# Kernel tuning notes

Measured on AMD Instinct MI355X. Metric: run time of the kernel, lower is better.

Reference implementation:

```python
import jax, jax.numpy as jnp
import numpy as np
import math

B, N, E = 256, 512, 2048          # graphs, nodes per graph, edges per graph
EMB = 64                           # emb_sz (must be 64 to match final per-graph matmul with 64-d fc2 output)
NUM_ITEMS, NUM_CATS = 400000, 1000
RATIO = 0.9
EPS = 1e-5


def _bn(x, g, b):
    # BatchNorm1d in training mode: biased batch statistics
    m = x.mean(axis=0)
    v = x.var(axis=0)
    return g * (x - m) * jax.lax.rsqrt(v + EPS) + b


def _graph_conv(x, src, dst, emask, Wr, Wn, b):
    # PyG GraphConv, aggr='add': out_i = lin_root(x_i) + lin_rel(sum_{j->i} x_j) + bias
    msg = jnp.where(emask[:, None], x[src], jnp.zeros((), x.dtype))  # [E_tot, C]
    agg = jnp.zeros_like(x).at[dst].add(msg)
    return agg @ Wn + x @ Wr + b


def _topk_pool(x, src, dst, emask, p, n):
    # TopKPooling: score = x.p/||p||, keep top ceil(ratio*n) per graph, gate with tanh(score)
    k = int(math.ceil(RATIO * n))
    score = x @ p / jnp.linalg.norm(p)                       # [B*n]
    _, idx = jax.lax.top_k(score.reshape(B, n), k)           # [B, k] local indices
    gidx = (idx + (jnp.arange(B) * n)[:, None]).reshape(-1)  # [B*k] global indices
    xk = x[gidx] * jnp.tanh(score[gidx])[:, None]
    # remap edges; edges touching a dropped node become masked-out
    mapping = jnp.full((B * n,), -1, jnp.int32).at[gidx].set(jnp.arange(B * k, dtype=jnp.int32))
    nsrc, ndst = mapping[src], mapping[dst]
    valid = (nsrc >= 0) & (ndst >= 0) & emask
    return xk, jnp.maximum(nsrc, 0), jnp.maximum(ndst, 0), valid, k


def _readout(x, k):
    # uniform graphs: global_max_pool / global_mean_pool via reshape
    xg = x.reshape(B, k, -1)
    return jnp.concatenate([xg.max(axis=1), xg.mean(axis=1)], axis=1)  # [B, 256]


def setup_inputs() -> dict:
    key = jax.random.key(0)
    ks = jax.random.split(key, 32)
    nrm = jax.random.normal
    s = 0.02
    item_id = jax.random.randint(ks[0], (B * N,), 0, NUM_ITEMS)
    cat_id = jax.random.randint(ks[1], (B * N,), 0, NUM_CATS)
    off = (jnp.arange(B, dtype=jnp.int32) * N)[:, None]
    src = (jax.random.randint(ks[2], (B, E), 0, N, dtype=jnp.int32) + off).reshape(-1)
    dst = (jax.random.randint(ks[3], (B, E), 0, N, dtype=jnp.int32) + off).reshape(-1)
    d = dict(
        item_id=item_id, cat_id=cat_id, src=src, dst=dst,
        emb_item=nrm(ks[4], (NUM_ITEMS, EMB)) * s,
        emb_cat=nrm(ks[5], (NUM_CATS, EMB)) * s,
        W1r=nrm(ks[6], (2 * EMB, 128)) * s, W1n=nrm(ks[7], (2 * EMB, 128)) * s, b1=jnp.zeros(128), p1=nrm(ks[8], (128,)),
        W2r=nrm(ks[9], (128, 128)) * s, W2n=nrm(ks[10], (128, 128)) * s, b2=jnp.zeros(128), p2=nrm(ks[11], (128,)),
        W3r=nrm(ks[12], (128, 128)) * s, W3n=nrm(ks[13], (128, 128)) * s, b3=jnp.zeros(128), p3=nrm(ks[14], (128,)),
        fc1_W=nrm(ks[15], (256, 128)) * s, fc1_b=jnp.zeros(128), bn1_g=jnp.ones(128), bn1_b=jnp.zeros(128),
        fc2_W=nrm(ks[16], (128, 64)) * s, fc2_b=jnp.zeros(64), bn2_g=jnp.ones(64), bn2_b=jnp.zeros(64),
    )
    return d


def reference(item_id, cat_id, src, dst, emb_item, emb_cat,
              W1r, W1n, b1, p1, W2r, W2n, b2, p2, W3r, W3n, b3, p3,
              fc1_W, fc1_b, bn1_g, bn1_b, fc2_W, fc2_b, bn2_g, bn2_b):
    e_item = emb_item[item_id]                               # [B*N, 64]
    e_cat = emb_cat[cat_id]                                  # [B*N, 64]
    x = jnp.concatenate([e_item, e_cat], axis=1)             # [B*N, 128]
    emask = jnp.ones(src.shape, bool)

    x = jax.nn.relu(_graph_conv(x, src, dst, emask, W1r, W1n, b1))
    x, src, dst, emask, k1 = _topk_pool(x, src, dst, emask, p1, N)
    x1 = _readout(x, k1)

    x = jax.nn.relu(_graph_conv(x, src, dst, emask, W2r, W2n, b2))
    x, src, dst, emask, k2 = _topk_pool(x, src, dst, emask, p2, k1)
    x2 = _readout(x, k2)

    x = jax.nn.relu(_graph_conv(x, src, dst, emask, W3r, W3n, b3))
    x, src, dst, emask, k3 = _topk_pool(x, src, dst, emask, p3, k2)
    x3 = _readout(x, k3)

    g = x1 + x2 + x3                                         # [B, 256]
    g = jax.nn.relu(_bn(g @ fc1_W + fc1_b, bn1_g, bn1_b))    # fc1
    g = jax.nn.relu(_bn(g @ fc2_W + fc2_b, bn2_g, bn2_b))    # fc2
    # dropout is identity in eval; original applies relu again after dropout
    g = jax.nn.relu(g)                                       # [B, 64]
    # per-graph matmul loop: out[n] = <emb_item[n], g[graph_of_n]>; uniform graphs -> einsum
    out = jnp.einsum('bnd,bd->bn', e_item.reshape(B, N, EMB), g).reshape(-1)
    return jax.nn.sigmoid(out)                               # [B*N]
```

## Files before the change

kernel.cpp:

```cpp
#include <hip/hip_runtime.h>
#include <hip/hip_bf16.h>
#include <math.h>


#define TOTAL_NODES 131072
#define NUM_GRAPHS  256
#define NODES_PER_G 512
#define E_TOTAL     524288
#define EPG         2048
#define FDIM        128
#define EMBD        64

typedef __bf16 bf16x8 __attribute__((ext_vector_type(8)));
typedef float  f32x4  __attribute__((ext_vector_type(4)));

static __device__ __forceinline__ f32x4 mfma16(bf16x8 a, bf16x8 b, f32x4 c) {
  return __builtin_amdgcn_mfma_f32_16x16x32_bf16(a, b, c, 0, 0, 0);
}

static inline size_t align256(size_t x) { return (x + 255) & ~size_t(255); }

__global__ __launch_bounds__(256) void gather_embed_k(
    const int* __restrict__ item_id, const int* __restrict__ cat_id,
    const float* __restrict__ emb_item, const float* __restrict__ emb_cat,
    float* __restrict__ x, int total)
{
  int i = blockIdx.x * 256 + threadIdx.x;
  int node = i >> 5, part = i & 31;
  if (node >= total) return;
  float4 v;
  if (part < 16) {
    v = *(const float4*)&emb_item[(size_t)item_id[node] * EMBD + part * 4];
  } else {
    v = *(const float4*)&emb_cat[(size_t)cat_id[node] * EMBD + (part - 16) * 4];
  }
  *(float4*)&x[(size_t)node * FDIM + part * 4] = v;
}

__global__ __launch_bounds__(256) void wprep_k(
    const float* __restrict__ w0, const float* __restrict__ w1,
    const float* __restrict__ w2, const float* __restrict__ w3,
    const float* __restrict__ w4, const float* __restrict__ w5,
    __bf16* __restrict__ wout)
{
  const float* ws[6] = {w0, w1, w2, w3, w4, w5};
  int mat = blockIdx.y;
  int idx = blockIdx.x * 256 + threadIdx.x;
  int n = idx >> 7, k = idx & 127;
  float v = ws[mat][k * FDIM + n];
  __bf16 h = (__bf16)v;
  __bf16 l = (__bf16)(v - (float)h);
  __bf16* base = wout + (size_t)mat * 2 * 16384;
  base[idx] = h;
  base[16384 + idx] = l;
}

__global__ __launch_bounds__(128) void pnorm3_k(
    const float* __restrict__ p1, const float* __restrict__ p2,
    const float* __restrict__ p3, float* __restrict__ nrm)
{
  __shared__ float ss[128];
  const float* ps[3] = {p1, p2, p3};
  int t = threadIdx.x;
  for (int m = 0; m < 3; ++m) {
    float v = ps[m][t];
    ss[t] = v * v;
    __syncthreads();
    for (int s = 64; s > 0; s >>= 1) {
      if (t < s) ss[t] += ss[t + s];
      __syncthreads();
    }
    if (t == 0) nrm[m] = sqrtf(ss[0]);
    __syncthreads();
  }
}

__global__ __launch_bounds__(512) void csr_build_k(
    const int* __restrict__ src_in, const int* __restrict__ dst_in,
    const int* __restrict__ mapping,
    const int* __restrict__ sel_,
    const float* __restrict__ gates_,
    int* __restrict__ src_out, int* __restrict__ dst_out,
    int2* __restrict__ slot_pack, int* __restrict__ counts,
    int* __restrict__ offs, int n_new)
{
  __shared__ int hist[512];
  __shared__ int scan[512];
  __shared__ int cursor[512];
  const int g = blockIdx.x, t = threadIdx.x;
  const int ebase = g * EPG;
  const int nbase = g * n_new;
  hist[t] = 0;
  __syncthreads();
  int ls[4], ld[4];
#pragma unroll
  for (int i = 0; i < 4; ++i) {
    int e = ebase + t + i * 512;
    int s = src_in[e], d = dst_in[e];
    if (mapping) {
      s = (s >= 0) ? mapping[s] : -1;
      d = (d >= 0) ? mapping[d] : -1;
      if (s < 0 || d < 0) { s = -1; d = -1; }
    }
    src_out[e] = s; dst_out[e] = d;
    ls[i] = (s >= 0) ? (s - nbase) : -1;
    ld[i] = (d >= 0) ? (d - nbase) : -1;
    if (ld[i] >= 0) atomicAdd(&hist[ld[i]], 1);
  }
  __syncthreads();
  int v = (t < n_new) ? hist[t] : 0;
  scan[t] = v;
  __syncthreads();
  for (int dlt = 1; dlt < 512; dlt <<= 1) {
    int add = (t >= dlt) ? scan[t - dlt] : 0;
    __syncthreads();
    scan[t] += add;
    __syncthreads();
  }
  if (t < n_new) {
    int excl = scan[t] - v;
    counts[nbase + t] = v;
    offs[nbase + t] = g * EPG + excl;
    cursor[t] = excl;
  }
  __syncthreads();
#pragma unroll
  for (int i = 0; i < 4; ++i) {
    if (ld[i] >= 0) {
      int pos = atomicAdd(&cursor[ld[i]], 1);
      int sg = nbase + ls[i];
      int oldr = sel_ ? sel_[sg] : sg;
      float gt = gates_ ? gates_[sg] : 1.0f;
      slot_pack[ebase + pos] = make_int2(oldr, __float_as_int(gt));
    }
  }
}

__global__ __launch_bounds__(256) void gather_direct_k(
    const float* __restrict__ x, const int2* __restrict__ slot_pack,
    const int* __restrict__ off, const int* __restrict__ counts,
    float* __restrict__ agg, int M)
{
  int i = blockIdx.x * 256 + threadIdx.x;
  int node = i >> 5, lane = i & 31;
  if (node >= M) return;
  int deg = counts[node];
  int base = off[node];
  float4 a = make_float4(0.f, 0.f, 0.f, 0.f);
  for (int d = 0; d < deg; ++d) {
    int2 sp = slot_pack[base + d];
    float gt = __int_as_float(sp.y);
    float4 v = *(const float4*)&x[(size_t)sp.x * FDIM + lane * 4];
    a.x += gt * v.x; a.y += gt * v.y; a.z += gt * v.z; a.w += gt * v.w;
  }
  *(float4*)&agg[(size_t)node * FDIM + lane * 4] = a;
}

__global__ __launch_bounds__(256) void conv_mfma_k(
    const float* __restrict__ Asrc, const int* __restrict__ sel,
    const float* __restrict__ gates,
    const __bf16* __restrict__ W1hl,
    const float* __restrict__ A2,
    const __bf16* __restrict__ W2hl,
    const float* __restrict__ bias, const float* __restrict__ p,
    const float* __restrict__ nrm, float* __restrict__ C,
    float* __restrict__ score, int M)
{
  __shared__ __bf16 Wh[128 * 72];
  __shared__ __bf16 Wl[128 * 72];

  const int tid  = threadIdx.x;
  const int lane = tid & 63;
  const int w    = tid >> 6;
  const int row0 = blockIdx.x * 128;
  const int l15  = lane & 15;
  const int lg   = lane >> 4;

  f32x4 acc[2][8];
#pragma unroll
  for (int rf = 0; rf < 2; ++rf)
#pragma unroll
    for (int cf = 0; cf < 8; ++cf) acc[rf][cf] = (f32x4){0.f, 0.f, 0.f, 0.f};

  const int grow0 = row0 + w * 32 + l15;
  const int grow1 = grow0 + 16;

  for (int pass = 0; pass < 2; ++pass) {
    const float* __restrict__ A = pass ? A2 : Asrc;
    const __bf16* __restrict__ Whl = pass ? W2hl : W1hl;
    const bool use_sel = (pass == 0) && (sel != nullptr);
    int srow0 = use_sel ? sel[grow0] : grow0;
    int srow1 = use_sel ? sel[grow1] : grow1;
    float gt0 = use_sel ? gates[grow0] : 1.0f;
    float gt1 = use_sel ? gates[grow1] : 1.0f;

    for (int half = 0; half < 2; ++half) {
      const int k0 = half * 64;
      __syncthreads();
      for (int v = tid; v < 1024; v += 256) {
        int c = v >> 3, chn = (v & 7) * 8;
        *(bf16x8*)&Wh[c * 72 + chn] = *(const bf16x8*)&Whl[c * 128 + k0 + chn];
        *(bf16x8*)&Wl[c * 72 + chn] = *(const bf16x8*)&Whl[16384 + c * 128 + k0 + chn];
      }
      __syncthreads();

      bf16x8 ah[2][2], al[2][2];
#pragma unroll
      for (int rf = 0; rf < 2; ++rf) {
        int srow = rf ? srow1 : srow0;
        float gt = rf ? gt1 : gt0;
#pragma unroll
        for (int kc = 0; kc < 2; ++kc) {
          const float* ap = &A[(size_t)srow * FDIM + k0 + kc * 32 + lg * 8];
          float4 u0 = *(const float4*)ap;
          float4 u1 = *(const float4*)(ap + 4);
          float av[8] = {u0.x, u0.y, u0.z, u0.w, u1.x, u1.y, u1.z, u1.w};
#pragma unroll
          for (int j = 0; j < 8; ++j) {
            float vv = av[j] * gt;
            __bf16 h = (__bf16)vv;
            ah[rf][kc][j] = h;
            al[rf][kc][j] = (__bf16)(vv - (float)h);
          }
        }
      }
#pragma unroll
      for (int kc = 0; kc < 2; ++kc) {
        const int koff = kc * 32 + lg * 8;
#pragma unroll
        for (int cf = 0; cf < 8; ++cf) {
          const int bo = (cf * 16 + l15) * 72 + koff;
          bf16x8 bh = *(const bf16x8*)&Wh[bo];
          bf16x8 bl = *(const bf16x8*)&Wl[bo];
          acc[0][cf] = mfma16(ah[0][kc], bh, acc[0][cf]);
          acc[0][cf] = mfma16(ah[0][kc], bl, acc[0][cf]);
          acc[0][cf] = mfma16(al[0][kc], bh, acc[0][cf]);
          acc[1][cf] = mfma16(ah[1][kc], bh, acc[1][cf]);
          acc[1][cf] = mfma16(ah[1][kc], bl, acc[1][cf]);
          acc[1][cf] = mfma16(al[1][kc], bh, acc[1][cf]);
        }
      }
    }
  }

  const float nv = nrm[0];
  float bv[8], pv[8];
#pragma unroll
  for (int cf = 0; cf < 8; ++cf) {
    int col = cf * 16 + l15;
    bv[cf] = bias[col];
    pv[cf] = p[col];
  }
#pragma unroll
  for (int rf = 0; rf < 2; ++rf) {
#pragma unroll
    for (int j = 0; j < 4; ++j) {
      int row = row0 + w * 32 + rf * 16 + lg * 4 + j;
      float* crow = &C[(size_t)row * FDIM];
      float rsv = 0.f;
#pragma unroll
      for (int cf = 0; cf < 8; ++cf) {
        float val = acc[rf][cf][j] + bv[cf];
        val = fmaxf(val, 0.f);
        crow[cf * 16 + l15] = val;
        rsv += val * pv[cf];
      }
      rsv += __shfl_xor(rsv, 1, 16);
      rsv += __shfl_xor(rsv, 2, 16);
      rsv += __shfl_xor(rsv, 4, 16);
      rsv += __shfl_xor(rsv, 8, 16);
      if (l15 == 0) score[row] = rsv / nv;
    }
  }
}

__global__ __launch_bounds__(512) void topk_sort_k(
    const float* __restrict__ score, int n_old, int k_new,
    int* __restrict__ sel, int* __restrict__ mapping, float* __restrict__ gates)
{
  __shared__ float sv[512];
  __shared__ int   si[512];
  int b = blockIdx.x, t = threadIdx.x;
  sv[t] = (t < n_old) ? -score[(size_t)b * n_old + t] : 3.0e38f;
  si[t] = t;
  __syncthreads();
  for (int k = 2; k <= 512; k <<= 1) {
    for (int j = k >> 1; j > 0; j >>= 1) {
      int ixj = t ^ j;
      if (ixj > t) {
        bool up = ((t & k) == 0);
        float a = sv[t], c = sv[ixj];
        if ((a > c) == up) {
          sv[t] = c; sv[ixj] = a;
          int tmp = si[t]; si[t] = si[ixj]; si[ixj] = tmp;
        }
      }
      __syncthreads();
    }
  }
  if (t < n_old) {
    int old_g = b * n_old + si[t];
    if (t < k_new) {
      sel[b * k_new + t] = old_g;
      mapping[old_g] = b * k_new + t;
      gates[b * k_new + t] = tanhf(-sv[t]);
    } else {
      mapping[old_g] = -1;
    }
  }
}

__global__ __launch_bounds__(256) void readout_k(
    const float* __restrict__ x, const int* __restrict__ sel,
    const float* __restrict__ gates, float* __restrict__ g, int k)
{
  __shared__ float lmx[32 * 36];
  __shared__ float lsm[32 * 36];
  const int b = blockIdx.x, ch = blockIdx.y;
  const int c0 = ch * 32;
  const int tid = threadIdx.x;
  const int lane = tid & 7;
  const int slot = tid >> 3;
  float4 mx = make_float4(-3.0e38f, -3.0e38f, -3.0e38f, -3.0e38f);
  float4 sm = make_float4(0.f, 0.f, 0.f, 0.f);
  for (int n = slot; n < k; n += 32) {
    int node = b * k + n;
    int old = sel[node];
    float gate = gates[node];
    float4 v = *(const float4*)&x[(size_t)old * FDIM + c0 + lane * 4];
    v.x *= gate; v.y *= gate; v.z *= gate; v.w *= gate;
    mx.x = fmaxf(mx.x, v.x); mx.y = fmaxf(mx.y, v.y);
    mx.z = fmaxf(mx.z, v.z); mx.w = fmaxf(mx.w, v.w);
    sm.x += v.x; sm.y += v.y; sm.z += v.z; sm.w += v.w;
  }
  float* pm = &lmx[slot * 36 + lane * 4];
  float* ps = &lsm[slot * 36 + lane * 4];
  pm[0] = mx.x; pm[1] = mx.y; pm[2] = mx.z; pm[3] = mx.w;
  ps[0] = sm.x; ps[1] = sm.y; ps[2] = sm.z; ps[3] = sm.w;
  __syncthreads();
  for (int s = 16; s > 0; s >>= 1) {
    if (slot < s) {
#pragma unroll
      for (int j = 0; j < 4; ++j) {
        int a = slot * 36 + lane * 4 + j;
        int bb = (slot + s) * 36 + lane * 4 + j;
        lmx[a] = fmaxf(lmx[a], lmx[bb]);
        lsm[a] += lsm[bb];
      }
    }
    __syncthreads();
  }
  if (slot == 0) {
    float inv_k = 1.f / (float)k;
#pragma unroll
    for (int j = 0; j < 4; ++j) {
      int c = c0 + lane * 4 + j;
      g[b * 256 + c]       += lmx[lane * 4 + j];
      g[b * 256 + 128 + c] += lsm[lane * 4 + j] * inv_k;
    }
  }
}

__global__ __launch_bounds__(256) void head1_k(
    const float* __restrict__ g, const float* __restrict__ W,
    const float* __restrict__ bias, const float* __restrict__ gamma,
    const float* __restrict__ beta, float* __restrict__ h1)
{
  __shared__ float wsl[256 * 8];
  __shared__ float rsum[256 * 9];
  __shared__ float rsq[256 * 9];
  const int c0 = blockIdx.x * 8;
  const int t = threadIdx.x;
#pragma unroll
  for (int j = 0; j < 8; ++j) wsl[t * 8 + j] = W[t * 128 + c0 + j];
  __syncthreads();
  float acc[8] = {0.f, 0.f, 0.f, 0.f, 0.f, 0.f, 0.f, 0.f};
  const float* grow = &g[t * 256];
#pragma unroll
  for (int k = 0; k < 256; k += 4) {
    float4 gv = *(const float4*)&grow[k];
#pragma unroll
    for (int j = 0; j < 8; ++j) {
      acc[j] += gv.x * wsl[(k + 0) * 8 + j] + gv.y * wsl[(k + 1) * 8 + j]
              + gv.z * wsl[(k + 2) * 8 + j] + gv.w * wsl[(k + 3) * 8 + j];
    }
  }
#pragma unroll
  for (int j = 0; j < 8; ++j) {
    acc[j] += bias[c0 + j];
    rsum[t * 9 + j] = acc[j];
    rsq[t * 9 + j] = acc[j] * acc[j];
  }
  __syncthreads();
  for (int s = 128; s > 0; s >>= 1) {
    if (t < s) {
#pragma unroll
      for (int j = 0; j < 8; ++j) {
        rsum[t * 9 + j] += rsum[(t + s) * 9 + j];
        rsq[t * 9 + j]  += rsq[(t + s) * 9 + j];
      }
    }
    __syncthreads();
  }
#pragma unroll
  for (int j = 0; j < 8; ++j) {
    float m = rsum[j] * (1.f / 256.f);
    float var = rsq[j] * (1.f / 256.f) - m * m;
    float o = gamma[c0 + j] * (acc[j] - m) * rsqrtf(var + 1e-5f) + beta[c0 + j];
    h1[t * 128 + c0 + j] = fmaxf(o, 0.f);
  }
}

__global__ __launch_bounds__(256) void head2_k(
    const float* __restrict__ h1, const float* __restrict__ W,
    const float* __restrict__ bias, const float* __restrict__ gamma,
    const float* __restrict__ beta, float* __restrict__ h2)
{
  __shared__ float wsl[128 * 8];
  __shared__ float rsum[256 * 9];
  __shared__ float rsq[256 * 9];
  const int c0 = blockIdx.x * 8;
  const int t = threadIdx.x;
  if (t < 128) {
#pragma unroll
    for (int j = 0; j < 8; ++j) wsl[t * 8 + j] = W[t * 64 + c0 + j];
  }
  __syncthreads();
  float acc[8] = {0.f, 0.f, 0.f, 0.f, 0.f, 0.f, 0.f, 0.f};
  const float* hrow = &h1[t * 128];
#pragma unroll
  for (int k = 0; k < 128; k += 4) {
    float4 gv = *(const float4*)&hrow[k];
#pragma unroll
    for (int j = 0; j < 8; ++j) {
      acc[j] += gv.x * wsl[(k + 0) * 8 + j] + gv.y * wsl[(k + 1) * 8 + j]
              + gv.z * wsl[(k + 2) * 8 + j] + gv.w * wsl[(k + 3) * 8 + j];
    }
  }
#pragma unroll
  for (int j = 0; j < 8; ++j) {
    acc[j] += bias[c0 + j];
    rsum[t * 9 + j] = acc[j];
    rsq[t * 9 + j] = acc[j] * acc[j];
  }
  __syncthreads();
  for (int s = 128; s > 0; s >>= 1) {
    if (t < s) {
#pragma unroll
      for (int j = 0; j < 8; ++j) {
        rsum[t * 9 + j] += rsum[(t + s) * 9 + j];
        rsq[t * 9 + j]  += rsq[(t + s) * 9 + j];
      }
    }
    __syncthreads();
  }
#pragma unroll
  for (int j = 0; j < 8; ++j) {
    float m = rsum[j] * (1.f / 256.f);
    float var = rsq[j] * (1.f / 256.f) - m * m;
    float o = gamma[c0 + j] * (acc[j] - m) * rsqrtf(var + 1e-5f) + beta[c0 + j];
    h2[t * 64 + c0 + j] = fmaxf(o, 0.f);
  }
}

__global__ __launch_bounds__(256) void final_k(
    const int* __restrict__ item_id, const float* __restrict__ emb_item,
    const float* __restrict__ g2, float* __restrict__ out, int total)
{
  int nid = blockIdx.x * 256 + threadIdx.x;
  if (nid >= total) return;
  int b = nid >> 9;
  const float* e = &emb_item[(size_t)item_id[nid] * EMBD];
  const float* gg = &g2[(size_t)b * 64];
  float s = 0.f;
#pragma unroll
  for (int j = 0; j < 64; j += 4) {
    float4 a = *(const float4*)&e[j];
    float4 c = *(const float4*)&gg[j];
    s += a.x * c.x + a.y * c.y + a.z * c.z + a.w * c.w;
  }
  out[nid] = 1.f / (1.f + expf(-s));
}

extern "C" void kernel_launch(void* const* d_in, const int* in_sizes, int n_in,
                              void* d_out, int out_size, void* d_ws, size_t ws_size,
                              hipStream_t stream)
{
  const int*   item_id  = (const int*)  d_in[0];
  const int*   cat_id   = (const int*)  d_in[1];
  const int*   src_in   = (const int*)  d_in[2];
  const int*   dst_in   = (const int*)  d_in[3];
  const float* emb_item = (const float*)d_in[4];
  const float* emb_cat  = (const float*)d_in[5];
  const float* W1r = (const float*)d_in[6];
  const float* W1n = (const float*)d_in[7];
  const float* b1  = (const float*)d_in[8];
  const float* p1  = (const float*)d_in[9];
  const float* W2r = (const float*)d_in[10];
  const float* W2n = (const float*)d_in[11];
  const float* b2  = (const float*)d_in[12];
  const float* p2  = (const float*)d_in[13];
  const float* W3r = (const float*)d_in[14];
  const float* W3n = (const float*)d_in[15];
  const float* b3  = (const float*)d_in[16];
  const float* p3  = (const float*)d_in[17];
  const float* fc1_W = (const float*)d_in[18];
  const float* fc1_b = (const float*)d_in[19];
  const float* bn1_g = (const float*)d_in[20];
  const float* bn1_b = (const float*)d_in[21];
  const float* fc2_W = (const float*)d_in[22];
  const float* fc2_b = (const float*)d_in[23];
  const float* bn2_g = (const float*)d_in[24];
  const float* bn2_b = (const float*)d_in[25];
  float* out = (float*)d_out;

  const int TN = TOTAL_NODES;
  const int E  = E_TOTAL;
  const int k1 = 461, k2 = 415, k3 = 374;
  const int M1 = TN;
  const int M2 = NUM_GRAPHS * k1;
  const int M3 = NUM_GRAPHS * k2;

  char* ws = (char*)d_ws;
  size_t off = 0;
  auto carve = [&](size_t bytes) { char* p = ws + off; off += align256(bytes); return p; };
  float*  buf0   = (float*) carve((size_t)TN * FDIM * 4);
  float*  buf1   = (float*) carve((size_t)TN * FDIM * 4);
  float*  score  = (float*) carve((size_t)TN * 4);
  int*    sel    = (int*)   carve((size_t)TN * 4);
  int*    mapping= (int*)   carve((size_t)TN * 4);
  float*  gates  = (float*) carve((size_t)TN * 4);
  int*    srcw   = (int*)   carve((size_t)E * 4);
  int*    dstw   = (int*)   carve((size_t)E * 4);
  int*    counts = (int*)   carve((size_t)TN * 4);
  int*    offs   = (int*)   carve((size_t)TN * 4);
  int2*   slotp  = (int2*)  carve((size_t)E * 8);
  __bf16* wbuf   = (__bf16*)carve(6 * 2 * 16384 * 2);
  float*  g      = (float*) carve(256 * 256 * 4);
  float*  h1     = (float*) carve(256 * 128 * 4);
  float*  h2     = (float*) carve(256 * 64 * 4);
  float*  nrm    = (float*) carve(256);
  if (off > ws_size) return;

  dim3 b256(256);
  auto blocks = [](long long work, int bs) { return dim3((unsigned)((work + bs - 1) / bs)); };

  const __bf16* W1r_hl = wbuf + 0 * 2 * 16384;
  const __bf16* W1n_hl = wbuf + 1 * 2 * 16384;
  const __bf16* W2r_hl = wbuf + 2 * 2 * 16384;
  const __bf16* W2n_hl = wbuf + 3 * 2 * 16384;
  const __bf16* W3r_hl = wbuf + 4 * 2 * 16384;
  const __bf16* W3n_hl = wbuf + 5 * 2 * 16384;

  hipMemsetAsync(g, 0, 256 * 256 * 4, stream);
  wprep_k<<<dim3(64, 6), b256, 0, stream>>>(W1r, W1n, W2r, W2n, W3r, W3n, wbuf);
  pnorm3_k<<<dim3(1), dim3(128), 0, stream>>>(p1, p2, p3, nrm);
  gather_embed_k<<<blocks((long long)TN * 32, 256), b256, 0, stream>>>(
      item_id, cat_id, emb_item, emb_cat, buf0, TN);

  csr_build_k<<<dim3(NUM_GRAPHS), dim3(512), 0, stream>>>(
      src_in, dst_in, nullptr, nullptr, nullptr,
      srcw, dstw, slotp, counts, offs, NODES_PER_G);
  gather_direct_k<<<blocks((long long)M1 * 32, 256), b256, 0, stream>>>(
      buf0, slotp, offs, counts, buf1, M1);
  conv_mfma_k<<<dim3(M1 / 128), b256, 0, stream>>>(
      buf0, nullptr, nullptr, W1r_hl, buf1, W1n_hl, b1, p1, nrm + 0, buf0, score, M1);
  topk_sort_k<<<dim3(NUM_GRAPHS), dim3(512), 0, stream>>>(
      score, NODES_PER_G, k1, sel, mapping, gates);
  readout_k<<<dim3(NUM_GRAPHS, 4), b256, 0, stream>>>(buf0, sel, gates, g, k1);

  csr_build_k<<<dim3(NUM_GRAPHS), dim3(512), 0, stream>>>(
      srcw, dstw, mapping, sel, gates,
      srcw, dstw, slotp, counts, offs, k1);
  gather_direct_k<<<blocks((long long)M2 * 32, 256), b256, 0, stream>>>(
      buf0, slotp, offs, counts, buf1, M2);
  conv_mfma_k<<<dim3(M2 / 128), b256, 0, stream>>>(
      buf0, sel, gates, W2r_hl, buf1, W2n_hl, b2, p2, nrm + 1, buf1, score, M2);
  topk_sort_k<<<dim3(NUM_GRAPHS), dim3(512), 0, stream>>>(
      score, k1, k2, sel, mapping, gates);
  readout_k<<<dim3(NUM_GRAPHS, 4), b256, 0, stream>>>(buf1, sel, gates, g, k2);

  csr_build_k<<<dim3(NUM_GRAPHS), dim3(512), 0, stream>>>(
      srcw, dstw, mapping, sel, gates,
      srcw, dstw, slotp, counts, offs, k2);
  gather_direct_k<<<blocks((long long)M3 * 32, 256), b256, 0, stream>>>(
      buf1, slotp, offs, counts, buf0, M3);
  conv_mfma_k<<<dim3(M3 / 128), b256, 0, stream>>>(
      buf1, sel, gates, W3r_hl, buf0, W3n_hl, b3, p3, nrm + 2, buf0, score, M3);
  topk_sort_k<<<dim3(NUM_GRAPHS), dim3(512), 0, stream>>>(
      score, k2, k3, sel, mapping, gates);
  readout_k<<<dim3(NUM_GRAPHS, 4), b256, 0, stream>>>(buf0, sel, gates, g, k3);

  head1_k<<<dim3(16), b256, 0, stream>>>(g, fc1_W, fc1_b, bn1_g, bn1_b, h1);
  head2_k<<<dim3(8), b256, 0, stream>>>(h1, fc2_W, fc2_b, bn2_g, bn2_b, h2);

  final_k<<<blocks(TN, 256), b256, 0, stream>>>(item_id, emb_item, h2, out, TN);
}
```

Before: 409.0 us.

## Fuse top-k, edge remap/CSR build and readout into one per-graph pool kernel

Merges the top-k sort, the next-level CSR construction and the max/mean readout into a single per-graph pool kernel. The node mapping and gates now stay in shared memory instead of a global mapping array. The first CSR build is specialised to skip the mapping logic. The final kernel reads item embeddings from the already gathered node features instead of re-gathering through item_id. This cuts kernel launches and global round trips, at the cost of extra feature buffers and a larger shared-memory footprint per block.

```diff
diff --git a/kernel.cpp b/kernel.cpp
--- a/kernel.cpp
+++ b/kernel.cpp
@@ -75,64 +75,50 @@
   }
 }
 
-__global__ __launch_bounds__(512) void csr_build_k(
+__global__ __launch_bounds__(512) void csr_build1_k(
     const int* __restrict__ src_in, const int* __restrict__ dst_in,
-    const int* __restrict__ mapping,
-    const int* __restrict__ sel_,
-    const float* __restrict__ gates_,
     int* __restrict__ src_out, int* __restrict__ dst_out,
-    int2* __restrict__ slot_pack, int* __restrict__ counts,
-    int* __restrict__ offs, int n_new)
+    int2* __restrict__ slot_pack, int* __restrict__ counts, int* __restrict__ offs)
 {
   __shared__ int hist[512];
-  __shared__ int scan[512];
-  __shared__ int cursor[512];
-  const int g = blockIdx.x, t = threadIdx.x;
-  const int ebase = g * EPG;
-  const int nbase = g * n_new;
+  __shared__ int scn[512];
+  __shared__ int cur[512];
+  const int b = blockIdx.x, t = threadIdx.x;
+  const int ebase = b * EPG;
+  const int nbase = b * NODES_PER_G;
   hist[t] = 0;
   __syncthreads();
-  int ls[4], ld[4];
+  int so[4], ld[4];
 #pragma unroll
   for (int i = 0; i < 4; ++i) {
     int e = ebase + t + i * 512;
-    int s = src_in[e], d = dst_in[e];
-    if (mapping) {
-      s = (s >= 0) ? mapping[s] : -1;
-      d = (d >= 0) ? mapping[d] : -1;
-      if (s < 0 || d < 0) { s = -1; d = -1; }
-    }
+    int s = src_in[e] - nbase;
+    int d = dst_in[e] - nbase;
     src_out[e] = s; dst_out[e] = d;
-    ls[i] = (s >= 0) ? (s - nbase) : -1;
-    ld[i] = (d >= 0) ? (d - nbase) : -1;
-    if (ld[i] >= 0) atomicAdd(&hist[ld[i]], 1);
-  }
-  __syncthreads();
-  int v = (t < n_new) ? hist[t] : 0;
-  scan[t] = v;
-  __syncthreads();
-  for (int dlt = 1; dlt < 512; dlt <<= 1) {
-    int add = (t >= dlt) ? scan[t - dlt] : 0;
-    __syncthreads();
-    scan[t] += add;
-    __syncthreads();
-  }
-  if (t < n_new) {
-    int excl = scan[t] - v;
+    so[i] = s; ld[i] = d;
+    atomicAdd(&hist[d], 1);
+  }
+  __syncthreads();
+  int v = hist[t];
+  scn[t] = v;
+  __syncthreads();
+  for (int dd = 1; dd < 512; dd <<= 1) {
+    int add = (t >= dd) ? scn[t - dd] : 0;
+    __syncthreads();
+    scn[t] += add;
+    __syncthreads();
+  }
+  {
+    int excl = scn[t] - v;
     counts[nbase + t] = v;
-    offs[nbase + t] = g * EPG + excl;
-    cursor[t] = excl;
+    offs[nbase + t] = ebase + excl;
+    cur[t] = excl;
   }
   __syncthreads();
 #pragma unroll
   for (int i = 0; i < 4; ++i) {
-    if (ld[i] >= 0) {
-      int pos = atomicAdd(&cursor[ld[i]], 1);
-      int sg = nbase + ls[i];
-      int oldr = sel_ ? sel_[sg] : sg;
-      float gt = gates_ ? gates_[sg] : 1.0f;
-      slot_pack[ebase + pos] = make_int2(oldr, __float_as_int(gt));
-    }
+    int pos = atomicAdd(&cur[ld[i]], 1);
+    slot_pack[ebase + pos] = make_int2(nbase + so[i], __float_as_int(1.0f));
   }
 }
 
@@ -274,21 +260,33 @@
   }
 }
 
-__global__ __launch_bounds__(512) void topk_sort_k(
-    const float* __restrict__ score, int n_old, int k_new,
-    int* __restrict__ sel, int* __restrict__ mapping, float* __restrict__ gates)
+__global__ __launch_bounds__(512) void pool_k(
+    const float* __restrict__ score, const float* __restrict__ x,
+    int n_old, int k_new,
+    int* __restrict__ sel, float* __restrict__ gates,
+    int* __restrict__ src_e, int* __restrict__ dst_e,
+    int2* __restrict__ slot_pack, int* __restrict__ counts,
+    int* __restrict__ offs, float* __restrict__ g)
 {
   __shared__ float sv[512];
   __shared__ int   si[512];
-  int b = blockIdx.x, t = threadIdx.x;
-  sv[t] = (t < n_old) ? -score[(size_t)b * n_old + t] : 3.0e38f;
+  __shared__ int   map_[512];
+  __shared__ float gl[512];
+  __shared__ int   hist[512];
+  __shared__ int   scn[512];
+  __shared__ int   cur[512];
+  __shared__ float rmx[4 * 128];
+  __shared__ float rsm[4 * 128];
+  const int b = blockIdx.x, t = threadIdx.x;
+  const int nbase = b * n_old;
+  sv[t] = (t < n_old) ? -score[nbase + t] : 3.0e38f;
   si[t] = t;
   __syncthreads();
-  for (int k = 2; k <= 512; k <<= 1) {
-    for (int j = k >> 1; j > 0; j >>= 1) {
+  for (int kk = 2; kk <= 512; kk <<= 1) {
+    for (int j = kk >> 1; j > 0; j >>= 1) {
       int ixj = t ^ j;
       if (ixj > t) {
-        bool up = ((t & k) == 0);
+        bool up = ((t & kk) == 0);
         float a = sv[t], c = sv[ixj];
         if ((a > c) == up) {
           sv[t] = c; sv[ixj] = a;
@@ -299,64 +297,79 @@
     }
   }
   if (t < n_old) {
-    int old_g = b * n_old + si[t];
+    int o = si[t];
     if (t < k_new) {
-      sel[b * k_new + t] = old_g;
-      mapping[old_g] = b * k_new + t;
-      gates[b * k_new + t] = tanhf(-sv[t]);
+      float gt = tanhf(-sv[t]);
+      sel[b * k_new + t] = nbase + o;
+      gates[b * k_new + t] = gt;
+      gl[t] = gt;
+      map_[o] = t;
     } else {
-      mapping[old_g] = -1;
-    }
-  }
-}
-
-__global__ __launch_bounds__(256) void readout_k(
-    const float* __restrict__ x, const int* __restrict__ sel,
-    const float* __restrict__ gates, float* __restrict__ g, int k)
-{
-  __shared__ float lmx[32 * 36];
-  __shared__ float lsm[32 * 36];
-  const int b = blockIdx.x, ch = blockIdx.y;
-  const int c0 = ch * 32;
-  const int tid = threadIdx.x;
-  const int lane = tid & 7;
-  const int slot = tid >> 3;
-  float4 mx = make_float4(-3.0e38f, -3.0e38f, -3.0e38f, -3.0e38f);
-  float4 sm = make_float4(0.f, 0.f, 0.f, 0.f);
-  for (int n = slot; n < k; n += 32) {
-    int node = b * k + n;
-    int old = sel[node];
-    float gate = gates[node];
-    float4 v = *(const float4*)&x[(size_t)old * FDIM + c0 + lane * 4];
-    v.x *= gate; v.y *= gate; v.z *= gate; v.w *= gate;
-    mx.x = fmaxf(mx.x, v.x); mx.y = fmaxf(mx.y, v.y);
-    mx.z = fmaxf(mx.z, v.z); mx.w = fmaxf(mx.w, v.w);
-    sm.x += v.x; sm.y += v.y; sm.z += v.z; sm.w += v.w;
-  }
-  float* pm = &lmx[slot * 36 + lane * 4];
-  float* ps = &lsm[slot * 36 + lane * 4];
-  pm[0] = mx.x; pm[1] = mx.y; pm[2] = mx.z; pm[3] = mx.w;
-  ps[0] = sm.x; ps[1] = sm.y; ps[2] = sm.z; ps[3] = sm.w;
-  __syncthreads();
-  for (int s = 16; s > 0; s >>= 1) {
-    if (slot < s) {
-#pragma unroll
-      for (int j = 0; j < 4; ++j) {
-        int a = slot * 36 + lane * 4 + j;
-        int bb = (slot + s) * 36 + lane * 4 + j;
-        lmx[a] = fmaxf(lmx[a], lmx[bb]);
-        lsm[a] += lsm[bb];
-      }
-    }
-    __syncthreads();
-  }
-  if (slot == 0) {
-    float inv_k = 1.f / (float)k;
-#pragma unroll
-    for (int j = 0; j < 4; ++j) {
-      int c = c0 + lane * 4 + j;
-      g[b * 256 + c]       += lmx[lane * 4 + j];
-      g[b * 256 + 128 + c] += lsm[lane * 4 + j] * inv_k;
+      map_[o] = -1;
+    }
+  }
+  __syncthreads();
+  if (slot_pack) {
+    hist[t] = 0;
+    __syncthreads();
+    const int ebase = b * EPG;
+    int so[4], ls[4], ld[4];
+#pragma unroll
+    for (int i = 0; i < 4; ++i) {
+      int e = ebase + t + i * 512;
+      int s = src_e[e], d = dst_e[e];
+      so[i] = s;
+      int ns = (s >= 0) ? map_[s] : -1;
+      int nd = (d >= 0) ? map_[d] : -1;
+      if (ns < 0 || nd < 0) { ns = -1; nd = -1; }
+      src_e[e] = ns; dst_e[e] = nd;
+      ls[i] = ns; ld[i] = nd;
+      if (nd >= 0) atomicAdd(&hist[nd], 1);
+    }
+    __syncthreads();
+    int v = (t < k_new) ? hist[t] : 0;
+    scn[t] = v;
+    __syncthreads();
+    for (int dd = 1; dd < 512; dd <<= 1) {
+      int add = (t >= dd) ? scn[t - dd] : 0;
+      __syncthreads();
+      scn[t] += add;
+      __syncthreads();
+    }
+    if (t < k_new) {
+      int excl = scn[t] - v;
+      counts[b * k_new + t] = v;
+      offs[b * k_new + t] = ebase + excl;
+      cur[t] = excl;
+    }
+    __syncthreads();
+#pragma unroll
+    for (int i = 0; i < 4; ++i) {
+      if (ld[i] >= 0) {
+        int pos = atomicAdd(&cur[ld[i]], 1);
+        slot_pack[ebase + pos] = make_int2(nbase + so[i], __float_as_int(gl[ls[i]]));
+      }
+    }
+  }
+  {
+    const int col = t & 127;
+    const int slot = t >> 7;
+    float mx = -3.0e38f, sm = 0.f;
+    for (int n = slot; n < k_new; n += 4) {
+      int old = nbase + si[n];
+      float v = x[(size_t)old * FDIM + col] * gl[n];
+      mx = fmaxf(mx, v);
+      sm += v;
+    }
+    rmx[slot * 128 + col] = mx;
+    rsm[slot * 128 + col] = sm;
+    __syncthreads();
+    if (slot == 0) {
+      float m0 = fmaxf(fmaxf(rmx[col], rmx[128 + col]),
+                       fmaxf(rmx[256 + col], rmx[384 + col]));
+      float s0 = rsm[col] + rsm[128 + col] + rsm[256 + col] + rsm[384 + col];
+      g[b * 256 + col]       += m0;
+      g[b * 256 + 128 + col] += s0 / (float)k_new;
     }
   }
 }
@@ -464,13 +477,13 @@
 }
 
 __global__ __launch_bounds__(256) void final_k(
-    const int* __restrict__ item_id, const float* __restrict__ emb_item,
-    const float* __restrict__ g2, float* __restrict__ out, int total)
+    const float* __restrict__ x0, const float* __restrict__ g2,
+    float* __restrict__ out, int total)
 {
   int nid = blockIdx.x * 256 + threadIdx.x;
   if (nid >= total) return;
   int b = nid >> 9;
-  const float* e = &emb_item[(size_t)item_id[nid] * EMBD];
+  const float* e = &x0[(size_t)nid * FDIM];
   const float* gg = &g2[(size_t)b * 64];
   float s = 0.f;
 #pragma unroll
@@ -524,11 +537,12 @@
   char* ws = (char*)d_ws;
   size_t off = 0;
   auto carve = [&](size_t bytes) { char* p = ws + off; off += align256(bytes); return p; };
-  float*  buf0   = (float*) carve((size_t)TN * FDIM * 4);
-  float*  buf1   = (float*) carve((size_t)TN * FDIM * 4);
+  float*  bufA   = (float*) carve((size_t)TN * FDIM * 4);
+  float*  bufB   = (float*) carve((size_t)TN * FDIM * 4);
+  float*  bufC   = (float*) carve((size_t)TN * FDIM * 4);
+  float*  bufD   = (float*) carve((size_t)TN * FDIM * 4);
   float*  score  = (float*) carve((size_t)TN * 4);
   int*    sel    = (int*)   carve((size_t)TN * 4);
-  int*    mapping= (int*)   carve((size_t)TN * 4);
   float*  gates  = (float*) carve((size_t)TN * 4);
   int*    srcw   = (int*)   carve((size_t)E * 4);
   int*    dstw   = (int*)   carve((size_t)E * 4);
@@ -556,43 +570,36 @@
   wprep_k<<<dim3(64, 6), b256, 0, stream>>>(W1r, W1n, W2r, W2n, W3r, W3n, wbuf);
   pnorm3_k<<<dim3(1), dim3(128), 0, stream>>>(p1, p2, p3, nrm);
   gather_embed_k<<<blocks((long long)TN * 32, 256), b256, 0, stream>>>(
-      item_id, cat_id, emb_item, emb_cat, buf0, TN);
-
-  csr_build_k<<<dim3(NUM_GRAPHS), dim3(512), 0, stream>>>(
-      src_in, dst_in, nullptr, nullptr, nullptr,
-      srcw, dstw, slotp, counts, offs, NODES_PER_G);
+      item_id, cat_id, emb_item, emb_cat, bufA, TN);
+
+  csr_build1_k<<<dim3(NUM_GRAPHS), dim3(512), 0, stream>>>(
+      src_in, dst_in, srcw, dstw, slotp, counts, offs);
   gather_direct_k<<<blocks((long long)M1 * 32, 256), b256, 0, stream>>>(
-      buf0, slotp, offs, counts, buf1, M1);
+      bufA, slotp, offs, counts, bufB, M1);
   conv_mfma_k<<<dim3(M1 / 128), b256, 0, stream>>>(
-      buf0, nullptr, nullptr, W1r_hl, buf1, W1n_hl, b1, p1, nrm + 0, buf0, score, M1);
-  topk_sort_k<<<dim3(NUM_GRAPHS), dim3(512), 0, stream>>>(
-      score, NODES_PER_G, k1, sel, mapping, gates);
-  readout_k<<<dim3(NUM_GRAPHS, 4), b256, 0, stream>>>(buf0, sel, gates, g, k1);
-
-  csr_build_k<<<dim3(NUM_GRAPHS), dim3(512), 0, stream>>>(
-      srcw, dstw, mapping, sel, gates,
-      srcw, dstw, slotp, counts, offs, k1);
+      bufA, nullptr, nullptr, W1r_hl, bufB, W1n_hl, b1, p1, nrm + 0, bufC, score, M1);
+  pool_k<<<dim3(NUM_GRAPHS), dim3(512), 0, stream>>>(
+      score, bufC, NODES_PER_G, k1, sel, gates, srcw, dstw,
+      slotp, counts, offs, g);
+
   gather_direct_k<<<blocks((long long)M2 * 32, 256), b256, 0, stream>>>(
-      buf0, slotp, offs, counts, buf1, M2);
+      bufC, slotp, offs, counts, bufB, M2);
   conv_mfma_k<<<dim3(M2 / 128), b256, 0, stream>>>(
-      buf0, sel, gates, W2r_hl, buf1, W2n_hl, b2, p2, nrm + 1, buf1, score, M2);
-  topk_sort_k<<<dim3(NUM_GRAPHS), dim3(512), 0, stream>>>(
-      score, k1, k2, sel, mapping, gates);
-  readout_k<<<dim3(NUM_GRAPHS, 4), b256, 0, stream>>>(buf1, sel, gates, g, k2);
-
-  csr_build_k<<<dim3(NUM_GRAPHS), dim3(512), 0, stream>>>(
-      srcw, dstw, mapping, sel, gates,
-      srcw, dstw, slotp, counts, offs, k2);
+      bufC, sel, gates, W2r_hl, bufB, W2n_hl, b2, p2, nrm + 1, bufD, score, M2);
+  pool_k<<<dim3(NUM_GRAPHS), dim3(512), 0, stream>>>(
+      score, bufD, k1, k2, sel, gates, srcw, dstw,
+      slotp, counts, offs, g);
+
   gather_direct_k<<<blocks((long long)M3 * 32, 256), b256, 0, stream>>>(
-      buf1, slotp, offs, counts, buf0, M3);
+      bufD, slotp, offs, counts, bufB, M3);
   conv_mfma_k<<<dim3(M3 / 128), b256, 0, stream>>>(
-      buf1, sel, gates, W3r_hl, buf0, W3n_hl, b3, p3, nrm + 2, buf0, score, M3);
-  topk_sort_k<<<dim3(NUM_GRAPHS), dim3(512), 0, stream>>>(
-      score, k2, k3, sel, mapping, gates);
-  readout_k<<<dim3(NUM_GRAPHS, 4), b256, 0, stream>>>(buf0, sel, gates, g, k3);
+      bufD, sel, gates, W3r_hl, bufB, W3n_hl, b3, p3, nrm + 2, bufC, score, M3);
+  pool_k<<<dim3(NUM_GRAPHS), dim3(512), 0, stream>>>(
+      score, bufC, k2, k3, sel, gates, nullptr, nullptr,
+      nullptr, nullptr, nullptr, g);
 
   head1_k<<<dim3(16), b256, 0, stream>>>(g, fc1_W, fc1_b, bn1_g, bn1_b, h1);
   head2_k<<<dim3(8), b256, 0, stream>>>(h1, fc2_W, fc2_b, bn2_g, bn2_b, h2);
 
-  final_k<<<blocks(TN, 256), b256, 0, stream>>>(item_id, emb_item, h2, out, TN);
-}
+  final_k<<<blocks(TN, 256), b256, 0, stream>>>(bufA, h2, out, TN);
+}
```

Result: slower. 494.3 us (+20.9%).

## Fuse neighbor aggregation into conv MFMA kernel and reuse gathered embeddings

Applied to the files above, without the earlier changes.

Removes the separate gather_direct_k kernel and computes the per-node neighbor sum directly inside conv_mfma_k's A-operand load for the neighbor pass, so the aggregated tensor is never written to or re-read from global memory. A third feature buffer is added so each conv reads and writes distinct buffers. The final kernel now reads item embeddings from the already-gathered x0 buffer (first 64 columns) instead of re-gathering from the embedding table. The trade-off is that the neighbor gather now runs twice per row (once for each K half) inside the MFMA kernel, with divergent degree loops that may stall the matrix pipeline.

```diff
diff --git a/kernel.cpp b/kernel.cpp
--- a/kernel.cpp
+++ b/kernel.cpp
@@ -136,32 +136,13 @@
   }
 }
 
-__global__ __launch_bounds__(256) void gather_direct_k(
-    const float* __restrict__ x, const int2* __restrict__ slot_pack,
-    const int* __restrict__ off, const int* __restrict__ counts,
-    float* __restrict__ agg, int M)
-{
-  int i = blockIdx.x * 256 + threadIdx.x;
-  int node = i >> 5, lane = i & 31;
-  if (node >= M) return;
-  int deg = counts[node];
-  int base = off[node];
-  float4 a = make_float4(0.f, 0.f, 0.f, 0.f);
-  for (int d = 0; d < deg; ++d) {
-    int2 sp = slot_pack[base + d];
-    float gt = __int_as_float(sp.y);
-    float4 v = *(const float4*)&x[(size_t)sp.x * FDIM + lane * 4];
-    a.x += gt * v.x; a.y += gt * v.y; a.z += gt * v.z; a.w += gt * v.w;
-  }
-  *(float4*)&agg[(size_t)node * FDIM + lane * 4] = a;
-}
-
 __global__ __launch_bounds__(256) void conv_mfma_k(
     const float* __restrict__ Asrc, const int* __restrict__ sel,
     const float* __restrict__ gates,
-    const __bf16* __restrict__ W1hl,
-    const float* __restrict__ A2,
-    const __bf16* __restrict__ W2hl,
+    const __bf16* __restrict__ Wr_hl,
+    const int2* __restrict__ slotp, const int* __restrict__ offs,
+    const int* __restrict__ counts,
+    const __bf16* __restrict__ Wn_hl,
     const float* __restrict__ bias, const float* __restrict__ p,
     const float* __restrict__ nrm, float* __restrict__ C,
     float* __restrict__ score, int M)
@@ -185,15 +166,15 @@
   const int grow0 = row0 + w * 32 + l15;
   const int grow1 = grow0 + 16;
 
+  const int  srow0 = sel ? sel[grow0] : grow0;
+  const int  srow1 = sel ? sel[grow1] : grow1;
+  const float gt0  = gates ? gates[grow0] : 1.0f;
+  const float gt1  = gates ? gates[grow1] : 1.0f;
+  const int deg0 = counts[grow0], base0 = offs[grow0];
+  const int deg1 = counts[grow1], base1 = offs[grow1];
+
   for (int pass = 0; pass < 2; ++pass) {
-    const float* __restrict__ A = pass ? A2 : Asrc;
-    const __bf16* __restrict__ Whl = pass ? W2hl : W1hl;
-    const bool use_sel = (pass == 0) && (sel != nullptr);
-    int srow0 = use_sel ? sel[grow0] : grow0;
-    int srow1 = use_sel ? sel[grow1] : grow1;
-    float gt0 = use_sel ? gates[grow0] : 1.0f;
-    float gt1 = use_sel ? gates[grow1] : 1.0f;
-
+    const __bf16* __restrict__ Whl = pass ? Wn_hl : Wr_hl;
     for (int half = 0; half < 2; ++half) {
       const int k0 = half * 64;
       __syncthreads();
@@ -207,17 +188,45 @@
       bf16x8 ah[2][2], al[2][2];
 #pragma unroll
       for (int rf = 0; rf < 2; ++rf) {
-        int srow = rf ? srow1 : srow0;
-        float gt = rf ? gt1 : gt0;
-#pragma unroll
-        for (int kc = 0; kc < 2; ++kc) {
-          const float* ap = &A[(size_t)srow * FDIM + k0 + kc * 32 + lg * 8];
+        float av[2][8];
+        if (pass == 0) {
+          int srow = rf ? srow1 : srow0;
+          float gt = rf ? gt1 : gt0;
+          const float* ap = &Asrc[(size_t)srow * FDIM + k0 + lg * 8];
           float4 u0 = *(const float4*)ap;
           float4 u1 = *(const float4*)(ap + 4);
-          float av[8] = {u0.x, u0.y, u0.z, u0.w, u1.x, u1.y, u1.z, u1.w};
+          float4 u2 = *(const float4*)(ap + 32);
+          float4 u3 = *(const float4*)(ap + 36);
+          av[0][0]=gt*u0.x; av[0][1]=gt*u0.y; av[0][2]=gt*u0.z; av[0][3]=gt*u0.w;
+          av[0][4]=gt*u1.x; av[0][5]=gt*u1.y; av[0][6]=gt*u1.z; av[0][7]=gt*u1.w;
+          av[1][0]=gt*u2.x; av[1][1]=gt*u2.y; av[1][2]=gt*u2.z; av[1][3]=gt*u2.w;
+          av[1][4]=gt*u3.x; av[1][5]=gt*u3.y; av[1][6]=gt*u3.z; av[1][7]=gt*u3.w;
+        } else {
+          int deg = rf ? deg1 : deg0;
+          int base = rf ? base1 : base0;
+#pragma unroll
+          for (int kc = 0; kc < 2; ++kc)
+#pragma unroll
+            for (int j = 0; j < 8; ++j) av[kc][j] = 0.f;
+          for (int d = 0; d < deg; ++d) {
+            int2 sp = slotp[base + d];
+            float gt = __int_as_float(sp.y);
+            const float* ap = &Asrc[(size_t)sp.x * FDIM + k0 + lg * 8];
+            float4 u0 = *(const float4*)ap;
+            float4 u1 = *(const float4*)(ap + 4);
+            float4 u2 = *(const float4*)(ap + 32);
+            float4 u3 = *(const float4*)(ap + 36);
+            av[0][0]+=gt*u0.x; av[0][1]+=gt*u0.y; av[0][2]+=gt*u0.z; av[0][3]+=gt*u0.w;
+            av[0][4]+=gt*u1.x; av[0][5]+=gt*u1.y; av[0][6]+=gt*u1.z; av[0][7]+=gt*u1.w;
+            av[1][0]+=gt*u2.x; av[1][1]+=gt*u2.y; av[1][2]+=gt*u2.z; av[1][3]+=gt*u2.w;
+            av[1][4]+=gt*u3.x; av[1][5]+=gt*u3.y; av[1][6]+=gt*u3.z; av[1][7]+=gt*u3.w;
+          }
+        }
+#pragma unroll
+        for (int kc = 0; kc < 2; ++kc) {
 #pragma unroll
           for (int j = 0; j < 8; ++j) {
-            float vv = av[j] * gt;
+            float vv = av[kc][j];
             __bf16 h = (__bf16)vv;
             ah[rf][kc][j] = h;
             al[rf][kc][j] = (__bf16)(vv - (float)h);
@@ -464,13 +473,13 @@
 }
 
 __global__ __launch_bounds__(256) void final_k(
-    const int* __restrict__ item_id, const float* __restrict__ emb_item,
-    const float* __restrict__ g2, float* __restrict__ out, int total)
+    const float* __restrict__ x0, const float* __restrict__ g2,
+    float* __restrict__ out, int total)
 {
   int nid = blockIdx.x * 256 + threadIdx.x;
   if (nid >= total) return;
   int b = nid >> 9;
-  const float* e = &emb_item[(size_t)item_id[nid] * EMBD];
+  const float* e = &x0[(size_t)nid * FDIM];
   const float* gg = &g2[(size_t)b * 64];
   float s = 0.f;
 #pragma unroll
@@ -524,8 +533,9 @@
   char* ws = (char*)d_ws;
   size_t off = 0;
   auto carve = [&](size_t bytes) { char* p = ws + off; off += align256(bytes); return p; };
-  float*  buf0   = (float*) carve((size_t)TN * FDIM * 4);
-  float*  buf1   = (float*) carve((size_t)TN * FDIM * 4);
+  float*  bufA   = (float*) carve((size_t)TN * FDIM * 4);
+  float*  bufB   = (float*) carve((size_t)TN * FDIM * 4);
+  float*  bufC   = (float*) carve((size_t)TN * FDIM * 4);
   float*  score  = (float*) carve((size_t)TN * 4);
   int*    sel    = (int*)   carve((size_t)TN * 4);
   int*    mapping= (int*)   carve((size_t)TN * 4);
@@ -556,43 +566,40 @@
   wprep_k<<<dim3(64, 6), b256, 0, stream>>>(W1r, W1n, W2r, W2n, W3r, W3n, wbuf);
   pnorm3_k<<<dim3(1), dim3(128), 0, stream>>>(p1, p2, p3, nrm);
   gather_embed_k<<<blocks((long long)TN * 32, 256), b256, 0, stream>>>(
-      item_id, cat_id, emb_item, emb_cat, buf0, TN);
+      item_id, cat_id, emb_item, emb_cat, bufA, TN);
 
   csr_build_k<<<dim3(NUM_GRAPHS), dim3(512), 0, stream>>>(
       src_in, dst_in, nullptr, nullptr, nullptr,
       srcw, dstw, slotp, counts, offs, NODES_PER_G);
-  gather_direct_k<<<blocks((long long)M1 * 32, 256), b256, 0, stream>>>(
-      buf0, slotp, offs, counts, buf1, M1);
   conv_mfma_k<<<dim3(M1 / 128), b256, 0, stream>>>(
-      buf0, nullptr, nullptr, W1r_hl, buf1, W1n_hl, b1, p1, nrm + 0, buf0, score, M1);
+      bufA, nullptr, nullptr, W1r_hl, slotp, offs, counts, W1n_hl,
+      b1, p1, nrm + 0, bufB, score, M1);
   topk_sort_k<<<dim3(NUM_GRAPHS), dim3(512), 0, stream>>>(
       score, NODES_PER_G, k1, sel, mapping, gates);
-  readout_k<<<dim3(NUM_GRAPHS, 4), b256, 0, stream>>>(buf0, sel, gates, g, k1);
+  readout_k<<<dim3(NUM_GRAPHS, 4), b256, 0, stream>>>(bufB, sel, gates, g, k1);
 
   csr_build_k<<<dim3(NUM_GRAPHS), dim3(512), 0, stream>>>(
       srcw, dstw, mapping, sel, gates,
       srcw, dstw, slotp, counts, offs, k1);
-  gather_direct_k<<<blocks((long long)M2 * 32, 256), b256, 0, stream>>>(
-      buf0, slotp, offs, counts, buf1, M2);
   conv_mfma_k<<<dim3(M2 / 128), b256, 0, stream>>>(
-      buf0, sel, gates, W2r_hl, buf1, W2n_hl, b2, p2, nrm + 1, buf1, score, M2);
+      bufB, sel, gates, W2r_hl, slotp, offs, counts, W2n_hl,
+      b2, p2, nrm + 1, bufC, score, M2);
   topk_sort_k<<<dim3(NUM_GRAPHS), dim3(512), 0, stream>>>(
       score, k1, k2, sel, mapping, gates);
-  readout_k<<<dim3(NUM_GRAPHS, 4), b256, 0, stream>>>(buf1, sel, gates, g, k2);
+  readout_k<<<dim3(NUM_GRAPHS, 4), b256, 0, stream>>>(bufC, sel, gates, g, k2);
 
   csr_build_k<<<dim3(NUM_GRAPHS), dim3(512), 0, stream>>>(
       srcw, dstw, mapping, sel, gates,
       srcw, dstw, slotp, counts, offs, k2);
-  gather_direct_k<<<blocks((long long)M3 * 32, 256), b256, 0, stream>>>(
-      buf1, slotp, offs, counts, buf0, M3);
   conv_mfma_k<<<dim3(M3 / 128), b256, 0, stream>>>(
-      buf1, sel, gates, W3r_hl, buf0, W3n_hl, b3, p3, nrm + 2, buf0, score, M3);
+      bufC, sel, gates, W3r_hl, slotp, offs, counts, W3n_hl,
+      b3, p3, nrm + 2, bufB, score, M3);
   topk_sort_k<<<dim3(NUM_GRAPHS), dim3(512), 0, stream>>>(
       score, k2, k3, sel, mapping, gates);
-  readout_k<<<dim3(NUM_GRAPHS, 4), b256, 0, stream>>>(buf0, sel, gates, g, k3);
+  readout_k<<<dim3(NUM_GRAPHS, 4), b256, 0, stream>>>(bufB, sel, gates, g, k3);
 
   head1_k<<<dim3(16), b256, 0, stream>>>(g, fc1_W, fc1_b, bn1_g, bn1_b, h1);
   head2_k<<<dim3(8), b256, 0, stream>>>(h1, fc2_W, fc2_b, bn2_g, bn2_b, h2);
 
-  final_k<<<blocks(TN, 256), b256, 0, stream>>>(item_id, emb_item, h2, out, TN);
-}
+  final_k<<<blocks(TN, 256), b256, 0, stream>>>(bufA, h2, out, TN);
+}
```

Result: slower. 428.5 us (+4.8%).
